# Performance work log

Hardware: AMD Instinct MI355X
Metric: run time of the kernel (lower is better)

## Reference

```python
import jax, jax.numpy as jnp
import numpy as np

PAD_ID, BOS_ID, EOS_ID = 0, 2, 3
NHEAD = 8


def _sincos(T, d):
    pos = jnp.arange(T, dtype=jnp.float32)
    omega = jnp.exp(-jnp.arange(0, d, 2, dtype=jnp.float32) * (np.log(10000.0) / d))
    out = pos[:, None] * omega[None, :]  # [T, d/2]
    return jnp.stack([jnp.sin(out), jnp.cos(out)], axis=2).reshape(T, d)[None]  # [1,T,d]


def _ln(x, g, b, eps=1e-5):
    mu = x.mean(-1, keepdims=True)
    var = ((x - mu) ** 2).mean(-1, keepdims=True)
    return (x - mu) / jnp.sqrt(var + eps) * g + b


def _mha(q_in, kv_in, wqkv, bqkv, wo, bo, mask):
    B, Tq, d = q_in.shape
    Tk = kv_in.shape[1]
    hd = d // NHEAD
    q = q_in @ wqkv[:d].T + bqkv[:d]
    k = kv_in @ wqkv[d:2 * d].T + bqkv[d:2 * d]
    v = kv_in @ wqkv[2 * d:].T + bqkv[2 * d:]
    q = q.reshape(B, Tq, NHEAD, hd).transpose(0, 2, 1, 3)
    k = k.reshape(B, Tk, NHEAD, hd).transpose(0, 2, 1, 3)
    v = v.reshape(B, Tk, NHEAD, hd).transpose(0, 2, 1, 3)
    s = jnp.einsum('bhqd,bhkd->bhqk', q, k) / np.sqrt(hd)
    if mask is not None:
        s = s + mask
    a = jax.nn.softmax(s, axis=-1)
    o = jnp.einsum('bhqk,bhkd->bhqd', a, v).transpose(0, 2, 1, 3).reshape(B, Tq, d)
    return o @ wo.T + bo


def _last_logits(tokens, state, emb_table, qkv_w, qkv_b, out_w, out_b,
                 ffn_w1, ffn_b1, ffn_w2, ffn_b2, ln_g, ln_b):
    T = tokens.shape[1]
    d = emb_table.shape[1]
    x = emb_table[tokens] * np.sqrt(d) + _sincos(T, d)
    mask = jnp.where(jnp.tril(jnp.ones((T, T), bool)), 0.0, -jnp.inf)
    L = qkv_w.shape[0]
    for l in range(L):
        x = _ln(x + _mha(x, x, qkv_w[l, 0], qkv_b[l, 0], out_w[l, 0], out_b[l, 0], mask), ln_g[l, 0], ln_b[l, 0])
        x = _ln(x + _mha(x, state, qkv_w[l, 1], qkv_b[l, 1], out_w[l, 1], out_b[l, 1], None), ln_g[l, 1], ln_b[l, 1])
        h = jax.nn.gelu(x @ ffn_w1[l].T + ffn_b1[l], approximate=False)
        x = _ln(x + h @ ffn_w2[l].T + ffn_b2[l], ln_g[l, 2], ln_b[l, 2])
    return x[:, -1, :] @ emb_table.T  # tied output projection


def setup_inputs() -> dict:
    key = jax.random.key(0)
    ks = jax.random.split(key, 8)
    V, d, L, dff, B, K = 32000, 512, 4, 2048, 8, 64
    s = 0.02
    emb = jax.random.normal(ks[1], (V, d), jnp.float32) * s
    emb = emb.at[PAD_ID].set(0.0)  # padding_idx row is zero
    return {
        'state': jax.random.normal(ks[0], (B, K, d), jnp.float32),
        'emb_table': emb,
        'qkv_w': jax.random.normal(ks[2], (L, 2, 3 * d, d), jnp.float32) * s,
        'qkv_b': jnp.zeros((L, 2, 3 * d), jnp.float32),
        'out_w': jax.random.normal(ks[3], (L, 2, d, d), jnp.float32) * s,
        'out_b': jnp.zeros((L, 2, d), jnp.float32),
        'ffn_w1': jax.random.normal(ks[4], (L, dff, d), jnp.float32) * s,
        'ffn_b1': jnp.zeros((L, dff), jnp.float32),
        'ffn_w2': jax.random.normal(ks[5], (L, d, dff), jnp.float32) * s,
        'ffn_b2': jnp.zeros((L, d), jnp.float32),
        'ln_g': jnp.ones((L, 3, d), jnp.float32),
        'ln_b': jnp.zeros((L, 3, d), jnp.float32),
        'max_length': 16,
        'top_k': 50,
    }


def reference(state, emb_table, qkv_w, qkv_b, out_w, out_b, ffn_w1, ffn_b1,
              ffn_w2, ffn_b2, ln_g, ln_b, max_length, top_k):
    B = state.shape[0]
    generated = jnp.full((B, 1), BOS_ID, dtype=jnp.int32)
    finished = jnp.zeros(B, dtype=bool)
    key = jax.random.key(1)
    temperature = 1.0
    for t in range(max_length):
        # faithful naive recompute: full self+cross attention over generated prefix
        logits = _last_logits(generated, state, emb_table, qkv_w, qkv_b, out_w, out_b,
                              ffn_w1, ffn_b1, ffn_w2, ffn_b2, ln_g, ln_b)
        logits = logits / max(temperature, 1e-8)
        thr = jax.lax.top_k(logits, top_k)[0][:, -1:]
        filt = jnp.where(logits < thr, -jnp.inf, logits)
        nxt = jax.random.categorical(jax.random.fold_in(key, t), filt, axis=-1)
        nxt = jnp.where(finished, PAD_ID, nxt).astype(jnp.int32)
        generated = jnp.concatenate([generated, nxt[:, None]], axis=1)
        finished = finished | (nxt == EOS_ID)
    return generated
```

## Files before the change

### kernel.cpp

```cpp
#include <hip/hip_runtime.h>
#include <math.h>
#include <stdint.h>

#define D     512
#define DFF   2048
#define BB    8
#define NB    2
#define NG    4
#define NH    8
#define HD    64
#define NV    32000
#define NL    4
#define TMAX  17
#define KC    64
#define STEPS 16
#define KTOP  50
#define PAD_ID 0
#define BOS_ID 2
#define EOS_ID 3
#define SCOPE __HIP_MEMORY_SCOPE_AGENT

__device__ __forceinline__ float ld1(const float* p) {
  return __hip_atomic_load(p, __ATOMIC_RELAXED, SCOPE);
}
__device__ __forceinline__ void st1(float* p, float v) {
  __hip_atomic_store(p, v, __ATOMIC_RELAXED, SCOPE);
}
__device__ __forceinline__ float2 ld2(const float* p) {
  union { double d; float2 f; } u;
  u.d = __hip_atomic_load((const double*)p, __ATOMIC_RELAXED, SCOPE);
  return u.f;
}
__device__ __forceinline__ unsigned ldu(const unsigned* p) {
  return __hip_atomic_load(p, __ATOMIC_RELAXED, SCOPE);
}

__device__ __forceinline__ void tf2x32(unsigned k0, unsigned k1, unsigned x0, unsigned x1,
                                       unsigned& o0, unsigned& o1)
{
  unsigned ks2 = k0 ^ k1 ^ 0x1BD11BDAu;
#define TFR(r) { x0 += x1; x1 = (x1 << (r)) | (x1 >> (32 - (r))); x1 ^= x0; }
  x0 += k0; x1 += k1;
  TFR(13) TFR(15) TFR(26) TFR(6)
  x0 += k1;  x1 += ks2 + 1u;
  TFR(17) TFR(29) TFR(16) TFR(24)
  x0 += ks2; x1 += k0 + 2u;
  TFR(13) TFR(15) TFR(26) TFR(6)
  x0 += k0;  x1 += k1 + 3u;
  TFR(17) TFR(29) TFR(16) TFR(24)
  x0 += k1;  x1 += ks2 + 4u;
  TFR(13) TFR(15) TFR(26) TFR(6)
  o0 = x0 + ks2; o1 = x1 + k0 + 5u;
#undef TFR
}

__device__ __forceinline__ float wredf(float v) {
  for (int o = 32; o; o >>= 1) v += __shfl_xor(v, o, 64);
  return v;
}
__device__ __forceinline__ float wredmaxf(float v) {
  for (int o = 32; o; o >>= 1) v = fmaxf(v, __shfl_xor(v, o, 64));
  return v;
}
__device__ __forceinline__ unsigned monok(float f) {
  unsigned u = __float_as_uint(f);
  return (u & 0x80000000u) ? ~u : (u | 0x80000000u);
}

#define DOT8(a0,a1,x0,x1) (a0.x*x0.x + a0.y*x0.y + a0.z*x0.z + a0.w*x0.w + \
                           a1.x*x1.x + a1.y*x1.y + a1.z*x1.z + a1.w*x1.w)

__global__ void init_k(int* toks, unsigned* bars)
{
  int i = threadIdx.x;
  if (i < BB) toks[i * TMAX] = BOS_ID;
  for (int k = i; k < 2048; k += 256) bars[k] = 0u;
}

__global__ void cross_kv_k(const float* __restrict__ state, const float* __restrict__ qkvw,
                           const float* __restrict__ qkvb, float* __restrict__ cK,
                           float* __restrict__ cV)
{
  int gx = blockIdx.x, b = blockIdx.y, tid = threadIdx.x;
  int jblk = gx & 31, kpos = (gx >> 5) & 63, l = gx >> 11;
  int w = tid >> 6, lane = tid & 63;
  __shared__ __align__(16) float xsh[D];
  xsh[tid] = state[((size_t)b * KC + kpos) * D + tid];
  xsh[tid + 256] = state[((size_t)b * KC + kpos) * D + tid + 256];
  __syncthreads();
  for (int i = 0; i < 8; i++) {
    int j = jblk * 32 + w * 8 + i;
    int row = D + j;
    const float4* wr = (const float4*)(qkvw + (((size_t)l * 2 + 1) * (3 * D) + row) * D);
    const float4* x4 = (const float4*)xsh;
    float acc = 0.f;
    for (int e = lane; e < 128; e += 64) {
      float4 a = wr[e], xx = x4[e];
      acc += a.x * xx.x + a.y * xx.y + a.z * xx.z + a.w * xx.w;
    }
    acc = wredf(acc);
    if (lane == 0) {
      float v = acc + qkvb[((size_t)l * 2 + 1) * (3 * D) + row];
      float* dst = (j < D) ? cK : cV;
      int jj = (j < D) ? j : j - D;
      dst[(((size_t)l * BB + b) * KC + kpos) * D + jj] = v;
    }
  }
}

extern "C" __global__ void __launch_bounds__(512, 2)
decode_k(const float* __restrict__ emb, const float* __restrict__ qkv_w,
         const float* __restrict__ qkv_b, const float* __restrict__ out_w,
         const float* __restrict__ out_b, const float* __restrict__ f_w1,
         const float* __restrict__ f_b1, const float* __restrict__ f_w2,
         const float* __restrict__ f_b2, const float* __restrict__ lng,
         const float* __restrict__ lnb,
         const float* __restrict__ cK, const float* __restrict__ cV,
         float* Kc, float* Vc, float* qS, float* q2S,
         float* xt2, float* xt3, float* xt4, float* hB,
         float* xcur, float* lg, unsigned* bars, int* toks)
{
  const int tid = threadIdx.x, bid = blockIdx.x;
  const int xcd = bid & 7;
  const int g2 = xcd >> 1;
  const int half = xcd & 1;
  const int hid = bid >> 3;
  const int gid = hid * 2 + half;
  const int sb = (gid + g2 * 16) & 63;
  const int b0 = g2 * 2, b1 = b0 + 1;
  const int w = tid >> 6, lane = tid & 63;
  const int wb = w >> 2;
  const int ws = w & 3;
  unsigned gp = 0, glp = 0;
  int finished = 0;

  __shared__ __align__(16) unsigned char smem[65280];
  float* F = (float*)smem;
  float* sX1 = F;
  float* sX2 = F + 1024;
  float* sQ  = F + 2048;
  float* sAO = F + 3072;
  float* sS  = F + 4096;
  float* sSP = F + 5184;
  float* sH  = F + 6272;
  float* sRed = F + 10368;
  float* sL  = F;
  unsigned short* key16 = (unsigned short*)smem;
  unsigned* histA = (unsigned*)(smem + 64000);
  unsigned* sKeys = (unsigned*)(smem + 64000);
  unsigned* sMeta = (unsigned*)(smem + 65024);
  float*    sWin  = (float*)(smem + 65056);
  int*      sWix  = (int*)(smem + 65120);

  const float SQD = (float)22.627416997969522;
  const float PEC = (float)(9.210340371976184 / 512.0);
  const float SQRT2 = (float)1.4142135623730951;

  auto gbarg = [&]() {
    asm volatile("s_waitcnt vmcnt(0)" ::: "memory");
    __syncthreads();
    ++gp;
    if (tid == 0) {
      unsigned* c = bars + g2 * 256;
      __hip_atomic_fetch_add(&c[(gid & 3) * 32], 1u, __ATOMIC_RELAXED, SCOPE);
      unsigned tgt = gp * 16u;
      if (gid == 0) {
        for (;;) {
          unsigned s0 = ldu(&c[0]), s1 = ldu(&c[32]), s2 = ldu(&c[64]), s3 = ldu(&c[96]);
          unsigned mn = s0 < s1 ? s0 : s1;
          unsigned mn2 = s2 < s3 ? s2 : s3;
          if ((mn < mn2 ? mn : mn2) >= tgt) break;
          __builtin_amdgcn_s_sleep(1);
        }
        __hip_atomic_store(&c[128], gp, __ATOMIC_RELAXED, SCOPE);
      } else {
        while (ldu(&c[128]) < gp) __builtin_amdgcn_s_sleep(1);
      }
    }
    asm volatile("" ::: "memory");
    __syncthreads();
  };
  auto gbarall = [&]() {
    asm volatile("s_waitcnt vmcnt(0)" ::: "memory");
    __syncthreads();
    ++glp;
    if (tid == 0) {
      unsigned* c = bars + 1024;
      __hip_atomic_fetch_add(&c[(bid & 15) * 32], 1u, __ATOMIC_RELAXED, SCOPE);
      unsigned tgt = glp * 16u;
      if (bid == 0) {
        for (;;) {
          unsigned mn = 0xFFFFFFFFu;
#pragma unroll
          for (int i = 0; i < 16; i++) { unsigned x = ldu(&c[i * 32]); mn = x < mn ? x : mn; }
          if (mn >= tgt) break;
          __builtin_amdgcn_s_sleep(1);
        }
        __hip_atomic_store(&c[576], glp, __ATOMIC_RELAXED, SCOPE);
      } else {
        while (ldu(&c[576]) < glp) __builtin_amdgcn_s_sleep(1);
      }
    }
    asm volatile("" ::: "memory");
    __syncthreads();
  };

  auto ln2 = [&](const float* srcbase, const float* gamma, const float* beta, float* dst) {
    int nb = tid >> 8, e = tid & 255;
    const float* sp = srcbase + (size_t)(b0 + nb) * D;
    float v0 = ld1(sp + e), v1 = ld1(sp + e + 256);
    float s = wredf(v0 + v1);
    if (lane == 0) sRed[w] = s;
    __syncthreads();
    float mu = (sRed[nb*4] + sRed[nb*4+1] + sRed[nb*4+2] + sRed[nb*4+3]) * (1.0f/512.0f);
    __syncthreads();
    float d0 = v0 - mu, d1 = v1 - mu;
    float q = wredf(d0*d0 + d1*d1);
    if (lane == 0) sRed[w] = q;
    __syncthreads();
    float sd = sqrtf((sRed[nb*4] + sRed[nb*4+1] + sRed[nb*4+2] + sRed[nb*4+3]) * (1.0f/512.0f) + 1e-5f);
    dst[nb*512 + e]       = d0 / sd * gamma[e]       + beta[e];
    dst[nb*512 + e + 256] = d1 / sd * gamma[e + 256] + beta[e + 256];
    __syncthreads();
  };

  if (bid < BB) {
    float pe = (tid & 1) ? 1.0f : 0.0f;
    st1(&xcur[bid * D + tid], emb[(size_t)BOS_ID * D + tid] * SQD + pe);
  }
  gbarg();

  for (int t = 0; t < STEPS; ++t) {
    const int T = t + 1;
    for (int l = 0; l < NL; ++l) {
      const float* wqkv0 = qkv_w + ((size_t)l * 2 + 0) * (3 * D) * D;
      const float* bqkv0 = qkv_b + ((size_t)l * 2 + 0) * (3 * D);
      const float* wqkv1 = qkv_w + ((size_t)l * 2 + 1) * (3 * D) * D;
      const float* bqkv1 = qkv_b + ((size_t)l * 2 + 1) * (3 * D);
      const float* wo0 = out_w + ((size_t)l * 2 + 0) * D * D;
      const float* bo0 = out_b + ((size_t)l * 2 + 0) * D;
      const float* wo1 = out_w + ((size_t)l * 2 + 1) * D * D;
      const float* bo1 = out_b + ((size_t)l * 2 + 1) * D;

      if (l == 0) {
        int nb = tid >> 8, e = tid & 255;
        sX1[nb*512 + e]       = ld1(&xcur[(b0 + nb) * D + e]);
        sX1[nb*512 + e + 256] = ld1(&xcur[(b0 + nb) * D + e + 256]);
        __syncthreads();
      } else {
        ln2(xt4, lng + ((size_t)(l - 1) * 3 + 2) * D, lnb + ((size_t)(l - 1) * 3 + 2) * D, sX1);
      }
      {
        const float4* xs4 = (const float4*)(sX1 + wb * 512);
        float4 x0 = xs4[lane], x1v = xs4[lane + 64];
        int jq = sb * 8 + ws * 2;
        int kvb = 512 + sb * 16 + ws * 4;
        float4 qa[2], qb[2], wa[4], wbv[4];
#pragma unroll
        for (int r = 0; r < 2; ++r) {
          const float4* w4 = (const float4*)(wqkv0 + (size_t)(jq + r) * D);
          qa[r] = w4[lane]; qb[r] = w4[lane + 64];
        }
#pragma unroll
        for (int r = 0; r < 4; ++r) {
          const float4* w4 = (const float4*)(wqkv0 + (size_t)(kvb + r) * D);
          wa[r] = w4[lane]; wbv[r] = w4[lane + 64];
        }
        float aq[2], ak[4];
#pragma unroll
        for (int r = 0; r < 2; ++r) aq[r] = DOT8(qa[r], qb[r], x0, x1v);
#pragma unroll
        for (int r = 0; r < 4; ++r) ak[r] = DOT8(wa[r], wbv[r], x0, x1v);
#pragma unroll
        for (int o = 32; o; o >>= 1) {
#pragma unroll
          for (int r = 0; r < 2; ++r) aq[r] += __shfl_xor(aq[r], o, 64);
#pragma unroll
          for (int r = 0; r < 4; ++r) ak[r] += __shfl_xor(ak[r], o, 64);
        }
        if (lane == 0) {
#pragma unroll
          for (int r = 0; r < 2; ++r) {
            int j = jq + r;
            st1(&qS[(size_t)(b0 + wb) * D + j], aq[r] + bqkv0[j]);
          }
#pragma unroll
          for (int r = 0; r < 4; ++r) {
            int j = kvb + r;
            float v = ak[r] + bqkv0[j];
            if (j < 1024)
              st1(&Kc[((((size_t)g2 * NL + l) * NB + wb) * TMAX + t) * D + (j - 512)], v);
            else
              st1(&Vc[((((size_t)g2 * NL + l) * NB + wb) * TMAX + t) * D + (j - 1024)], v);
          }
        }
      }
      gbarg();

      {
        int nb = tid >> 8, e = tid & 255;
        sQ[nb*512 + e]       = ld1(&qS[(b0 + nb) * D + e]);
        sQ[nb*512 + e + 256] = ld1(&qS[(b0 + nb) * D + e + 256]);
      }
      __syncthreads();
      for (int o = tid; o < NB * NH * TMAX; o += 512) {
        int nb = o / (NH * TMAX), rem = o - nb * (NH * TMAX);
        int h = rem / TMAX, k = rem - h * TMAX;
        if (k < T) {
          const float4* Kr = (const float4*)(Kc + ((((size_t)g2 * NL + l) * NB + nb) * TMAX + k) * D + h * HD);
          const float4* q4 = (const float4*)(sQ + nb * 512 + h * HD);
          float sc = 0.f;
#pragma unroll
          for (int e = 0; e < 16; ++e) {
            float4 a = Kr[e], b2 = q4[e];
            sc += a.x * b2.x + a.y * b2.y + a.z * b2.z + a.w * b2.w;
          }
          sS[nb * 544 + h * TMAX + k] = sc * 0.125f;
        }
      }
      __syncthreads();
      for (int rr = w; rr < 16; rr += 8) {
        int nb = rr >> 3, h = rr & 7;
        float v = (lane < T) ? sS[nb * 544 + h * TMAX + lane] : -INFINITY;
        float m = wredmaxf(v);
        float p = (lane < T) ? expf(v - m) : 0.f;
        float den = wredf(p);
        if (lane < T) sSP[nb * 544 + h * TMAX + lane] = p / den;
      }
      __syncthreads();
      for (int o = tid; o < 1024; o += 512) {
        int nb = o >> 9, dd = o & 511, h = dd >> 6, d3 = dd & 63;
        const float* Vb = Vc + ((((size_t)g2 * NL + l) * NB + nb) * TMAX) * D + h * HD + d3;
        float acc = 0.f;
        for (int k = 0; k < T; ++k) acc += sSP[nb * 544 + h * TMAX + k] * Vb[(size_t)k * D];
        sAO[nb * 512 + dd] = acc;
      }
      __syncthreads();
      {
        int jb = sb * 8 + ws * 2;
        const float4* yN = (const float4*)(sAO + wb * 512);
        float4 y0 = yN[lane], y1 = yN[lane + 64];
        float acc[2];
#pragma unroll
        for (int r = 0; r < 2; ++r) {
          const float4* w4 = (const float4*)(wo0 + (size_t)(jb + r) * D);
          float4 a0 = w4[lane], a1 = w4[lane + 64];
          acc[r] = DOT8(a0, a1, y0, y1);
        }
#pragma unroll
        for (int o = 32; o; o >>= 1) {
#pragma unroll
          for (int r = 0; r < 2; ++r) acc[r] += __shfl_xor(acc[r], o, 64);
        }
        if (lane == 0) {
#pragma unroll
          for (int r = 0; r < 2; ++r) {
            int j = jb + r;
            st1(&xt2[(size_t)(b0 + wb) * D + j], acc[r] + bo0[j] + sX1[wb * 512 + j]);
          }
        }
      }
      gbarg();

      ln2(xt2, lng + ((size_t)l * 3 + 0) * D, lnb + ((size_t)l * 3 + 0) * D, sX2);
      {
        int jb = sb * 8 + ws * 2;
        const float4* yN = (const float4*)(sX2 + wb * 512);
        float4 y0 = yN[lane], y1 = yN[lane + 64];
        float acc[2];
#pragma unroll
        for (int r = 0; r < 2; ++r) {
          const float4* w4 = (const float4*)(wqkv1 + (size_t)(jb + r) * D);
          float4 a0 = w4[lane], a1 = w4[lane + 64];
          acc[r] = DOT8(a0, a1, y0, y1);
        }
#pragma unroll
        for (int o = 32; o; o >>= 1) {
#pragma unroll
          for (int r = 0; r < 2; ++r) acc[r] += __shfl_xor(acc[r], o, 64);
        }
        if (lane == 0) {
#pragma unroll
          for (int r = 0; r < 2; ++r) {
            int j = jb + r;
            st1(&q2S[(size_t)(b0 + wb) * D + j], acc[r] + bqkv1[j]);
          }
        }
      }
      gbarg();

      {
        int nb = tid >> 8, e = tid & 255;
        sQ[nb*512 + e]       = ld1(&q2S[(b0 + nb) * D + e]);
        sQ[nb*512 + e + 256] = ld1(&q2S[(b0 + nb) * D + e + 256]);
      }
      __syncthreads();
      for (int o = tid; o < 1024; o += 512) {
        int nb = o >> 9, dd = o & 511, h = dd >> 6, k = dd & 63;
        const float4* Kr = (const float4*)(cK + (((size_t)l * BB + b0 + nb) * KC + k) * D + h * HD);
        const float4* q4 = (const float4*)(sQ + nb * 512 + h * HD);
        float sc = 0.f;
#pragma unroll
        for (int e = 0; e < 16; ++e) {
          float4 a = Kr[e], b2 = q4[e];
          sc += a.x * b2.x + a.y * b2.y + a.z * b2.z + a.w * b2.w;
        }
        sS[nb * 512 + dd] = sc * 0.125f;
      }
      __syncthreads();
      for (int rr = w; rr < 16; rr += 8) {
        int nb = rr >> 3, h = rr & 7;
        float v = sS[nb * 512 + h * 64 + lane];
        float m = wredmaxf(v);
        float p = expf(v - m);
        float den = wredf(p);
        sSP[nb * 512 + h * 64 + lane] = p / den;
      }
      __syncthreads();
      for (int o = tid; o < 1024; o += 512) {
        int nb = o >> 9, dd = o & 511, h = dd >> 6, d3 = dd & 63;
        const float* Vb = cV + (((size_t)l * BB + b0 + nb) * KC) * D + h * HD + d3;
        float acc = 0.f;
        for (int k = 0; k < KC; ++k) acc += sSP[nb * 512 + h * 64 + k] * Vb[(size_t)k * D];
        sAO[nb * 512 + dd] = acc;
      }
      __syncthreads();
      {
        int jb = sb * 8 + ws * 2;
        const float4* yN = (const float4*)(sAO + wb * 512);
        float4 y0 = yN[lane], y1 = yN[lane + 64];
        float acc[2];
#pragma unroll
        for (int r = 0; r < 2; ++r) {
          const float4* w4 = (const float4*)(wo1 + (size_t)(jb + r) * D);
          float4 a0 = w4[lane], a1 = w4[lane + 64];
          acc[r] = DOT8(a0, a1, y0, y1);
        }
#pragma unroll
        for (int o = 32; o; o >>= 1) {
#pragma unroll
          for (int r = 0; r < 2; ++r) acc[r] += __shfl_xor(acc[r], o, 64);
        }
        if (lane == 0) {
#pragma unroll
          for (int r = 0; r < 2; ++r) {
            int j = jb + r;
            st1(&xt3[(size_t)(b0 + wb) * D + j], acc[r] + bo1[j] + sX2[wb * 512 + j]);
          }
        }
      }
      gbarg();

      ln2(xt3, lng + ((size_t)l * 3 + 1) * D, lnb + ((size_t)l * 3 + 1) * D, sX1);
      {
        const float4* xs4 = (const float4*)(sX1 + wb * 512);
        float4 x0 = xs4[lane], x1v = xs4[lane + 64];
        for (int pass = 0; pass < 2; ++pass) {
          int jb = sb * 32 + ws * 8 + pass * 4;
          float4 wa[4], wbv[4];
#pragma unroll
          for (int r = 0; r < 4; ++r) {
            const float4* w4 = (const float4*)(f_w1 + (size_t)l * DFF * D + (size_t)(jb + r) * D);
            wa[r] = w4[lane]; wbv[r] = w4[lane + 64];
          }
          float acc[4];
#pragma unroll
          for (int r = 0; r < 4; ++r) acc[r] = DOT8(wa[r], wbv[r], x0, x1v);
#pragma unroll
          for (int o = 32; o; o >>= 1) {
#pragma unroll
            for (int r = 0; r < 4; ++r) acc[r] += __shfl_xor(acc[r], o, 64);
          }
          if (lane == 0) {
#pragma unroll
            for (int r = 0; r < 4; ++r) {
              int j = jb + r;
              float v = acc[r] + f_b1[(size_t)l * DFF + j];
              v = v * (erff(v / SQRT2) + 1.0f) / 2.0f;
              st1(&hB[(size_t)(b0 + wb) * DFF + j], v);
            }
          }
        }
      }
      gbarg();

      for (int ii = tid; ii < 2048; ii += 512) {
        int nbb = ii >> 10, ee = (ii & 1023) * 2;
        float2 v = ld2(&hB[(size_t)(b0 + nbb) * DFF + ee]);
        sH[nbb * 2048 + ee] = v.x; sH[nbb * 2048 + ee + 1] = v.y;
      }
      __syncthreads();
      {
        int jb = sb * 8 + ws * 2;
        const float4* hN = (const float4*)(sH + wb * 2048);
        float acc[2];
#pragma unroll
        for (int r = 0; r < 2; ++r) {
          const float4* w4 = (const float4*)(f_w2 + (size_t)l * D * DFF + (size_t)(jb + r) * DFF);
          float a = 0.f;
#pragma unroll
          for (int e = 0; e < 8; ++e) {
            float4 aw0 = w4[lane + e * 64];
            float4 hh0 = hN[lane + e * 64];
            a += aw0.x * hh0.x + aw0.y * hh0.y + aw0.z * hh0.z + aw0.w * hh0.w;
          }
          acc[r] = a;
        }
#pragma unroll
        for (int o = 32; o; o >>= 1) {
#pragma unroll
          for (int r = 0; r < 2; ++r) acc[r] += __shfl_xor(acc[r], o, 64);
        }
        if (lane == 0) {
#pragma unroll
          for (int r = 0; r < 2; ++r) {
            int j = jb + r;
            st1(&xt4[(size_t)(b0 + wb) * D + j], acc[r] + f_b2[(size_t)l * D + j] + sX1[wb * 512 + j]);
          }
        }
      }
      if (l < NL - 1) gbarg(); else gbarall();
    }

    for (int ii = tid; ii < 2048; ii += 512) {
      float2 v = ld2(&xt4[2 * ii]);
      sL[2 * ii] = v.x; sL[2 * ii + 1] = v.y;
    }
    __syncthreads();
    {
      int b = w;
      float vals[8]; float s = 0.f;
#pragma unroll
      for (int e = 0; e < 8; ++e) { vals[e] = sL[b * D + lane + e * 64]; s += vals[e]; }
      s = wredf(s);
      float mu = s * (1.0f / 512.0f);
      float q = 0.f;
#pragma unroll
      for (int e = 0; e < 8; ++e) { float d0 = vals[e] - mu; q += d0 * d0; }
      q = wredf(q);
      float sd = sqrtf(q * (1.0f / 512.0f) + 1e-5f);
      const float* ga = lng + 11 * D;
      const float* be = lnb + 11 * D;
#pragma unroll
      for (int e = 0; e < 8; ++e)
        sL[b * D + lane + e * 64] = (vals[e] - mu) / sd * ga[lane + e * 64] + be[lane + e * 64];
    }
    __syncthreads();
    for (int i = w; i < 125; i += 8) {
      int v = i * 256 + bid;
      const float4* er = (const float4*)(emb + (size_t)v * D);
      float4 e0 = er[lane], e1 = er[lane + 64];
      float acc[8];
#pragma unroll
      for (int b = 0; b < 8; b++) {
        const float4* x4 = (const float4*)(sL + b * D);
        float4 x0 = x4[lane], x1v = x4[lane + 64];
        acc[b] = DOT8(e0, e1, x0, x1v);
      }
#pragma unroll
      for (int o = 32; o; o >>= 1) {
#pragma unroll
        for (int b = 0; b < 8; b++) acc[b] += __shfl_xor(acc[b], o, 64);
      }
      if (lane == 0) {
#pragma unroll
        for (int b = 0; b < 8; b++) st1(&lg[(size_t)b * NV + v], acc[b]);
      }
    }
    gbarall();

    if (bid < BB) {
      int b = bid;
      if (tid < 256) histA[tid] = 0u;
      __syncthreads();
      for (int v2 = tid; v2 < NV / 2; v2 += 512) {
        float2 f = ld2(&lg[(size_t)b * NV + 2 * v2]);
        unsigned u0 = monok(f.x), u1 = monok(f.y);
        key16[2 * v2] = (unsigned short)(u0 >> 16);
        key16[2 * v2 + 1] = (unsigned short)(u1 >> 16);
        atomicAdd(&histA[u0 >> 24], 1u);
        atomicAdd(&histA[u1 >> 24], 1u);
      }
      __syncthreads();
      if (tid == 0) {
        unsigned k = KTOP, cum = 0;
        for (int bin = 255; bin >= 0; bin--) {
          cum += histA[bin];
          if (cum >= k) { sMeta[0] = (unsigned)bin; sMeta[1] = k - (cum - histA[bin]); break; }
        }
      }
      __syncthreads();
      unsigned selHi = sMeta[0], rem1 = sMeta[1];
      if (tid < 256) histA[tid] = 0u;
      __syncthreads();
      for (int v = tid; v < NV; v += 512) {
        unsigned k16 = key16[v];
        if ((k16 >> 8) == selHi) atomicAdd(&histA[k16 & 255u], 1u);
      }
      __syncthreads();
      if (tid == 0) {
        unsigned k = rem1, cum = 0;
        for (int bin = 255; bin >= 0; bin--) {
          cum += histA[bin];
          if (cum >= k) { sMeta[2] = (selHi << 8) | (unsigned)bin; sMeta[1] = k - (cum - histA[bin]); break; }
        }
        sMeta[3] = 0u;
      }
      __syncthreads();
      unsigned P16 = sMeta[2], rem2 = sMeta[1];
      for (int v = tid; v < NV; v += 512) {
        if (key16[v] == (unsigned short)P16) {
          unsigned i = atomicAdd(&sMeta[3], 1u);
          if (i < 256) sKeys[i] = monok(ld1(&lg[(size_t)b * NV + v]));
        }
      }
      __syncthreads();
      if (tid == 0) {
        unsigned n = sMeta[3]; if (n > 256) n = 256;
        unsigned thr = 0;
        for (unsigned it = 0; it < rem2; ++it) {
          unsigned bestk = 0; int bj = 0;
          for (unsigned jx = 0; jx < n; jx++)
            if (sKeys[jx] > bestk) { bestk = sKeys[jx]; bj = (int)jx; }
          thr = bestk;
          sKeys[bj] = 0u;
        }
        sMeta[5] = (thr & 0x80000000u) ? (thr ^ 0x80000000u) : ~thr;
      }
      __syncthreads();
      float th = __uint_as_float(sMeta[5]);
      unsigned k0, k1;
      tf2x32(0u, 1u, 0u, (unsigned)t, k0, k1);
      float best = -INFINITY; int bi = NV;
      for (int v = tid; v < NV; v += 512) {
        if (key16[v] >= (unsigned short)P16) {
          float lo = ld1(&lg[(size_t)b * NV + v]);
          if (lo >= th) {
            unsigned o0, o1;
            tf2x32(k0, k1, 0u, (unsigned)(b * NV + v), o0, o1);
            unsigned bits = o0 ^ o1;
            unsigned ub = (bits >> 9) | 0x3f800000u;
            float fu = __uint_as_float(ub) - 1.0f;
            const float TINY = 1.17549435e-38f;
            float u = fu * (1.0f - TINY) + TINY;
            u = fmaxf(TINY, u);
            float gmb = -logf(-logf(u));
            float s = lo + gmb;
            if (s > best || (s == best && v < bi)) { best = s; bi = v; }
          }
        }
      }
      for (int o = 32; o; o >>= 1) {
        float ob = __shfl_xor(best, o, 64); int ox = __shfl_xor(bi, o, 64);
        if (ob > best || (ob == best && ox < bi)) { best = ob; bi = ox; }
      }
      if (lane == 0) { sWin[w] = best; sWix[w] = bi; }
      __syncthreads();
      if (tid == 0) {
        float bb = sWin[0]; int bx = sWix[0];
        for (int i2 = 1; i2 < 8; i2++) {
          if (sWin[i2] > bb || (sWin[i2] == bb && sWix[i2] < bx)) { bb = sWin[i2]; bx = sWix[i2]; }
        }
        int tok = bx;
        if (finished) tok = PAD_ID;
        toks[b * TMAX + t + 1] = tok;
        if (tok == EOS_ID) finished = 1;
        sMeta[4] = (unsigned)tok;
      }
      __syncthreads();
      {
        int tok = (int)sMeta[4];
        float omega = expf(-(float)(tid & ~1) * PEC);
        float val = (float)(t + 1) * omega;
        float pe = (tid & 1) ? cosf(val) : sinf(val);
        st1(&xcur[b * D + tid], emb[(size_t)tok * D + tid] * SQD + pe);
      }
    }
    gbarg();
  }
}

extern "C" void kernel_launch(void* const* d_in, const int* in_sizes, int n_in,
                              void* d_out, int out_size, void* d_ws, size_t ws_size,
                              hipStream_t stream)
{
  const float* state = (const float*)d_in[0];
  const float* emb   = (const float*)d_in[1];
  const float* qkv_w = (const float*)d_in[2];
  const float* qkv_b = (const float*)d_in[3];
  const float* out_w = (const float*)d_in[4];
  const float* out_b = (const float*)d_in[5];
  const float* f_w1  = (const float*)d_in[6];
  const float* f_b1  = (const float*)d_in[7];
  const float* f_w2  = (const float*)d_in[8];
  const float* f_b2  = (const float*)d_in[9];
  const float* lng   = (const float*)d_in[10];
  const float* lnb   = (const float*)d_in[11];

  float* ws = (float*)d_ws;
  float* cK   = ws;
  float* cV   = cK + (size_t)NL * BB * KC * D;
  float* Kc   = cV + (size_t)NL * BB * KC * D;
  float* Vc   = Kc + (size_t)8 * NL * NB * TMAX * D;
  float* qS   = Vc + (size_t)8 * NL * NB * TMAX * D;
  float* q2S  = qS + BB * D;
  float* xt2  = q2S + BB * D;
  float* xt3  = xt2 + BB * D;
  float* xt4  = xt3 + BB * D;
  float* hB   = xt4 + BB * D;
  float* xcur = hB + BB * DFF;
  float* lg   = xcur + BB * D;
  unsigned* bars = (unsigned*)(lg + (size_t)BB * NV);

  int* toks = (int*)d_out;

  init_k<<<1, 256, 0, stream>>>(toks, bars);
  cross_kv_k<<<dim3(NL * KC * 32, BB), 256, 0, stream>>>(state, qkv_w, qkv_b, cK, cV);
  decode_k<<<256, 512, 0, stream>>>(emb, qkv_w, qkv_b, out_w, out_b,
                                    f_w1, f_b1, f_w2, f_b2, lng, lnb,
                                    cK, cV, Kc, Vc, qS, q2S,
                                    xt2, xt3, xt4, hB, xcur, lg, bars, toks);
}
```

Measured before the change: 4.960 ms.

## Prefetch stage weights before barrier-dependent work and spin without sleep

Each stage's weight rows (QKV, out-proj, FFN first pass) are now loaded into registers before the LayerNorm, attention, or activation reads that depend on the preceding grid barrier. The global-memory weight latency can then overlap with the reductions and attention math. The grid barrier spin loops also drop s_sleep, to cut wake-up latency at each barrier. The cost is higher register pressure and more polling traffic on the barrier counters.

```diff
diff --git a/kernel.cpp b/kernel.cpp
--- a/kernel.cpp
+++ b/kernel.cpp
@@ -170,11 +170,10 @@
           unsigned mn = s0 < s1 ? s0 : s1;
           unsigned mn2 = s2 < s3 ? s2 : s3;
           if ((mn < mn2 ? mn : mn2) >= tgt) break;
-          __builtin_amdgcn_s_sleep(1);
         }
         __hip_atomic_store(&c[128], gp, __ATOMIC_RELAXED, SCOPE);
       } else {
-        while (ldu(&c[128]) < gp) __builtin_amdgcn_s_sleep(1);
+        while (ldu(&c[128]) < gp) {}
       }
     }
     asm volatile("" ::: "memory");
@@ -194,11 +193,10 @@
 #pragma unroll
           for (int i = 0; i < 16; i++) { unsigned x = ldu(&c[i * 32]); mn = x < mn ? x : mn; }
           if (mn >= tgt) break;
-          __builtin_amdgcn_s_sleep(1);
         }
         __hip_atomic_store(&c[576], glp, __ATOMIC_RELAXED, SCOPE);
       } else {
-        while (ldu(&c[576]) < glp) __builtin_amdgcn_s_sleep(1);
+        while (ldu(&c[576]) < glp) {}
       }
     }
     asm volatile("" ::: "memory");
@@ -242,17 +240,7 @@
       const float* wo1 = out_w + ((size_t)l * 2 + 1) * D * D;
       const float* bo1 = out_b + ((size_t)l * 2 + 1) * D;
 
-      if (l == 0) {
-        int nb = tid >> 8, e = tid & 255;
-        sX1[nb*512 + e]       = ld1(&xcur[(b0 + nb) * D + e]);
-        sX1[nb*512 + e + 256] = ld1(&xcur[(b0 + nb) * D + e + 256]);
-        __syncthreads();
-      } else {
-        ln2(xt4, lng + ((size_t)(l - 1) * 3 + 2) * D, lnb + ((size_t)(l - 1) * 3 + 2) * D, sX1);
-      }
       {
-        const float4* xs4 = (const float4*)(sX1 + wb * 512);
-        float4 x0 = xs4[lane], x1v = xs4[lane + 64];
         int jq = sb * 8 + ws * 2;
         int kvb = 512 + sb * 16 + ws * 4;
         float4 qa[2], qb[2], wa[4], wbv[4];
@@ -266,6 +254,16 @@
           const float4* w4 = (const float4*)(wqkv0 + (size_t)(kvb + r) * D);
           wa[r] = w4[lane]; wbv[r] = w4[lane + 64];
         }
+        if (l == 0) {
+          int nb = tid >> 8, e = tid & 255;
+          sX1[nb*512 + e]       = ld1(&xcur[(b0 + nb) * D + e]);
+          sX1[nb*512 + e + 256] = ld1(&xcur[(b0 + nb) * D + e + 256]);
+          __syncthreads();
+        } else {
+          ln2(xt4, lng + ((size_t)(l - 1) * 3 + 2) * D, lnb + ((size_t)(l - 1) * 3 + 2) * D, sX1);
+        }
+        const float4* xs4 = (const float4*)(sX1 + wb * 512);
+        float4 x0 = xs4[lane], x1v = xs4[lane + 64];
         float aq[2], ak[4];
 #pragma unroll
         for (int r = 0; r < 2; ++r) aq[r] = DOT8(qa[r], qb[r], x0, x1v);
@@ -298,16 +296,118 @@
       gbarg();
 
       {
-        int nb = tid >> 8, e = tid & 255;
-        sQ[nb*512 + e]       = ld1(&qS[(b0 + nb) * D + e]);
-        sQ[nb*512 + e + 256] = ld1(&qS[(b0 + nb) * D + e + 256]);
-      }
-      __syncthreads();
-      for (int o = tid; o < NB * NH * TMAX; o += 512) {
-        int nb = o / (NH * TMAX), rem = o - nb * (NH * TMAX);
-        int h = rem / TMAX, k = rem - h * TMAX;
-        if (k < T) {
-          const float4* Kr = (const float4*)(Kc + ((((size_t)g2 * NL + l) * NB + nb) * TMAX + k) * D + h * HD);
+        int jb = sb * 8 + ws * 2;
+        float4 oa[2], ob[2];
+#pragma unroll
+        for (int r = 0; r < 2; ++r) {
+          const float4* w4 = (const float4*)(wo0 + (size_t)(jb + r) * D);
+          oa[r] = w4[lane]; ob[r] = w4[lane + 64];
+        }
+        {
+          int nb = tid >> 8, e = tid & 255;
+          sQ[nb*512 + e]       = ld1(&qS[(b0 + nb) * D + e]);
+          sQ[nb*512 + e + 256] = ld1(&qS[(b0 + nb) * D + e + 256]);
+        }
+        __syncthreads();
+        for (int o = tid; o < NB * NH * TMAX; o += 512) {
+          int nb = o / (NH * TMAX), rem = o - nb * (NH * TMAX);
+          int h = rem / TMAX, k = rem - h * TMAX;
+          if (k < T) {
+            const float4* Kr = (const float4*)(Kc + ((((size_t)g2 * NL + l) * NB + nb) * TMAX + k) * D + h * HD);
+            const float4* q4 = (const float4*)(sQ + nb * 512 + h * HD);
+            float sc = 0.f;
+#pragma unroll
+            for (int e = 0; e < 16; ++e) {
+              float4 a = Kr[e], b2 = q4[e];
+              sc += a.x * b2.x + a.y * b2.y + a.z * b2.z + a.w * b2.w;
+            }
+            sS[nb * 544 + h * TMAX + k] = sc * 0.125f;
+          }
+        }
+        __syncthreads();
+        for (int rr = w; rr < 16; rr += 8) {
+          int nb = rr >> 3, h = rr & 7;
+          float v = (lane < T) ? sS[nb * 544 + h * TMAX + lane] : -INFINITY;
+          float m = wredmaxf(v);
+          float p = (lane < T) ? expf(v - m) : 0.f;
+          float den = wredf(p);
+          if (lane < T) sSP[nb * 544 + h * TMAX + lane] = p / den;
+        }
+        __syncthreads();
+        for (int o = tid; o < 1024; o += 512) {
+          int nb = o >> 9, dd = o & 511, h = dd >> 6, d3 = dd & 63;
+          const float* Vb = Vc + ((((size_t)g2 * NL + l) * NB + nb) * TMAX) * D + h * HD + d3;
+          float acc = 0.f;
+          for (int k = 0; k < T; ++k) acc += sSP[nb * 544 + h * TMAX + k] * Vb[(size_t)k * D];
+          sAO[nb * 512 + dd] = acc;
+        }
+        __syncthreads();
+        const float4* yN = (const float4*)(sAO + wb * 512);
+        float4 y0 = yN[lane], y1 = yN[lane + 64];
+        float acc[2];
+#pragma unroll
+        for (int r = 0; r < 2; ++r) acc[r] = DOT8(oa[r], ob[r], y0, y1);
+#pragma unroll
+        for (int o = 32; o; o >>= 1) {
+#pragma unroll
+          for (int r = 0; r < 2; ++r) acc[r] += __shfl_xor(acc[r], o, 64);
+        }
+        if (lane == 0) {
+#pragma unroll
+          for (int r = 0; r < 2; ++r) {
+            int j = jb + r;
+            st1(&xt2[(size_t)(b0 + wb) * D + j], acc[r] + bo0[j] + sX1[wb * 512 + j]);
+          }
+        }
+      }
+      gbarg();
+
+      {
+        int jb = sb * 8 + ws * 2;
+        float4 qa[2], qb[2];
+#pragma unroll
+        for (int r = 0; r < 2; ++r) {
+          const float4* w4 = (const float4*)(wqkv1 + (size_t)(jb + r) * D);
+          qa[r] = w4[lane]; qb[r] = w4[lane + 64];
+        }
+        ln2(xt2, lng + ((size_t)l * 3 + 0) * D, lnb + ((size_t)l * 3 + 0) * D, sX2);
+        const float4* yN = (const float4*)(sX2 + wb * 512);
+        float4 y0 = yN[lane], y1 = yN[lane + 64];
+        float acc[2];
+#pragma unroll
+        for (int r = 0; r < 2; ++r) acc[r] = DOT8(qa[r], qb[r], y0, y1);
+#pragma unroll
+        for (int o = 32; o; o >>= 1) {
+#pragma unroll
+          for (int r = 0; r < 2; ++r) acc[r] += __shfl_xor(acc[r], o, 64);
+        }
+        if (lane == 0) {
+#pragma unroll
+          for (int r = 0; r < 2; ++r) {
+            int j = jb + r;
+            st1(&q2S[(size_t)(b0 + wb) * D + j], acc[r] + bqkv1[j]);
+          }
+        }
+      }
+      gbarg();
+
+      {
+        int jb = sb * 8 + ws * 2;
+        float4 oa[2], ob[2];
+#pragma unroll
+        for (int r = 0; r < 2; ++r) {
+          const float4* w4 = (const float4*)(wo1 + (size_t)(jb + r) * D);
+          oa[r] = w4[lane]; ob[r] = w4[lane + 64];
+        }
+        {
+          int nb = tid >> 8, e = tid & 255;
+          sQ[nb*512 + e]       = ld1(&q2S[(b0 + nb) * D + e]);
+          sQ[nb*512 + e + 256] = ld1(&q2S[(b0 + nb) * D + e + 256]);
+        }
+        __syncthreads();
+        for (int o = tid; o < 1024; o += 512) {
+          int nb = o >> 9, dd = o & 511, h = dd >> 6, k = dd & 63;
+          const float4* Kr = (const float4*)(cK + (((size_t)l * BB + b0 + nb) * KC + k) * D + h * HD);
           const float4* q4 = (const float4*)(sQ + nb * 512 + h * HD);
           float sc = 0.f;
 #pragma unroll
@@ -315,127 +415,31 @@
             float4 a = Kr[e], b2 = q4[e];
             sc += a.x * b2.x + a.y * b2.y + a.z * b2.z + a.w * b2.w;
           }
-          sS[nb * 544 + h * TMAX + k] = sc * 0.125f;
-        }
-      }
-      __syncthreads();
-      for (int rr = w; rr < 16; rr += 8) {
-        int nb = rr >> 3, h = rr & 7;
-        float v = (lane < T) ? sS[nb * 544 + h * TMAX + lane] : -INFINITY;
-        float m = wredmaxf(v);
-        float p = (lane < T) ? expf(v - m) : 0.f;
-        float den = wredf(p);
-        if (lane < T) sSP[nb * 544 + h * TMAX + lane] = p / den;
-      }
-      __syncthreads();
-      for (int o = tid; o < 1024; o += 512) {
-        int nb = o >> 9, dd = o & 511, h = dd >> 6, d3 = dd & 63;
-        const float* Vb = Vc + ((((size_t)g2 * NL + l) * NB + nb) * TMAX) * D + h * HD + d3;
-        float acc = 0.f;
-        for (int k = 0; k < T; ++k) acc += sSP[nb * 544 + h * TMAX + k] * Vb[(size_t)k * D];
-        sAO[nb * 512 + dd] = acc;
-      }
-      __syncthreads();
-      {
-        int jb = sb * 8 + ws * 2;
+          sS[nb * 512 + dd] = sc * 0.125f;
+        }
+        __syncthreads();
+        for (int rr = w; rr < 16; rr += 8) {
+          int nb = rr >> 3, h = rr & 7;
+          float v = sS[nb * 512 + h * 64 + lane];
+          float m = wredmaxf(v);
+          float p = expf(v - m);
+          float den = wredf(p);
+          sSP[nb * 512 + h * 64 + lane] = p / den;
+        }
+        __syncthreads();
+        for (int o = tid; o < 1024; o += 512) {
+          int nb = o >> 9, dd = o & 511, h = dd >> 6, d3 = dd & 63;
+          const float* Vb = cV + (((size_t)l * BB + b0 + nb) * KC) * D + h * HD + d3;
+          float acc = 0.f;
+          for (int k = 0; k < KC; ++k) acc += sSP[nb * 512 + h * 64 + k] * Vb[(size_t)k * D];
+          sAO[nb * 512 + dd] = acc;
+        }
+        __syncthreads();
         const float4* yN = (const float4*)(sAO + wb * 512);
         float4 y0 = yN[lane], y1 = yN[lane + 64];
         float acc[2];
 #pragma unroll
-        for (int r = 0; r < 2; ++r) {
-          const float4* w4 = (const float4*)(wo0 + (size_t)(jb + r) * D);
-          float4 a0 = w4[lane], a1 = w4[lane + 64];
-          acc[r] = DOT8(a0, a1, y0, y1);
-        }
-#pragma unroll
-        for (int o = 32; o; o >>= 1) {
-#pragma unroll
-          for (int r = 0; r < 2; ++r) acc[r] += __shfl_xor(acc[r], o, 64);
-        }
-        if (lane == 0) {
-#pragma unroll
-          for (int r = 0; r < 2; ++r) {
-            int j = jb + r;
-            st1(&xt2[(size_t)(b0 + wb) * D + j], acc[r] + bo0[j] + sX1[wb * 512 + j]);
-          }
-        }
-      }
-      gbarg();
-
-      ln2(xt2, lng + ((size_t)l * 3 + 0) * D, lnb + ((size_t)l * 3 + 0) * D, sX2);
-      {
-        int jb = sb * 8 + ws * 2;
-        const float4* yN = (const float4*)(sX2 + wb * 512);
-        float4 y0 = yN[lane], y1 = yN[lane + 64];
-        float acc[2];
-#pragma unroll
-        for (int r = 0; r < 2; ++r) {
-          const float4* w4 = (const float4*)(wqkv1 + (size_t)(jb + r) * D);
-          float4 a0 = w4[lane], a1 = w4[lane + 64];
-          acc[r] = DOT8(a0, a1, y0, y1);
-        }
-#pragma unroll
-        for (int o = 32; o; o >>= 1) {
-#pragma unroll
-          for (int r = 0; r < 2; ++r) acc[r] += __shfl_xor(acc[r], o, 64);
-        }
-        if (lane == 0) {
-#pragma unroll
-          for (int r = 0; r < 2; ++r) {
-            int j = jb + r;
-            st1(&q2S[(size_t)(b0 + wb) * D + j], acc[r] + bqkv1[j]);
-          }
-        }
-      }
-      gbarg();
-
-      {
-        int nb = tid >> 8, e = tid & 255;
-        sQ[nb*512 + e]       = ld1(&q2S[(b0 + nb) * D + e]);
-        sQ[nb*512 + e + 256] = ld1(&q2S[(b0 + nb) * D + e + 256]);
-      }
-      __syncthreads();
-      for (int o = tid; o < 1024; o += 512) {
-        int nb = o >> 9, dd = o & 511, h = dd >> 6, k = dd & 63;
-        const float4* Kr = (const float4*)(cK + (((size_t)l * BB + b0 + nb) * KC + k) * D + h * HD);
-        const float4* q4 = (const float4*)(sQ + nb * 512 + h * HD);
-        float sc = 0.f;
-#pragma unroll
-        for (int e = 0; e < 16; ++e) {
-          float4 a = Kr[e], b2 = q4[e];
-          sc += a.x * b2.x + a.y * b2.y + a.z * b2.z + a.w * b2.w;
-        }
-        sS[nb * 512 + dd] = sc * 0.125f;
-      }
-      __syncthreads();
-      for (int rr = w; rr < 16; rr += 8) {
-        int nb = rr >> 3, h = rr & 7;
-        float v = sS[nb * 512 + h * 64 + lane];
-        float m = wredmaxf(v);
-        float p = expf(v - m);
-        float den = wredf(p);
-        sSP[nb * 512 + h * 64 + lane] = p / den;
-      }
-      __syncthreads();
-      for (int o = tid; o < 1024; o += 512) {
-        int nb = o >> 9, dd = o & 511, h = dd >> 6, d3 = dd & 63;
-        const float* Vb = cV + (((size_t)l * BB + b0 + nb) * KC) * D + h * HD + d3;
-        float acc = 0.f;
-        for (int k = 0; k < KC; ++k) acc += sSP[nb * 512 + h * 64 + k] * Vb[(size_t)k * D];
-        sAO[nb * 512 + dd] = acc;
-      }
-      __syncthreads();
-      {
-        int jb = sb * 8 + ws * 2;
-        const float4* yN = (const float4*)(sAO + wb * 512);
-        float4 y0 = yN[lane], y1 = yN[lane + 64];
-        float acc[2];
-#pragma unroll
-        for (int r = 0; r < 2; ++r) {
-          const float4* w4 = (const float4*)(wo1 + (size_t)(jb + r) * D);
-          float4 a0 = w4[lane], a1 = w4[lane + 64];
-          acc[r] = DOT8(a0, a1, y0, y1);
-        }
+        for (int r = 0; r < 2; ++r) acc[r] = DOT8(oa[r], ob[r], y0, y1);
 #pragma unroll
         for (int o = 32; o; o >>= 1) {
 #pragma unroll
@@ -451,12 +455,38 @@
       }
       gbarg();
 
-      ln2(xt3, lng + ((size_t)l * 3 + 1) * D, lnb + ((size_t)l * 3 + 1) * D, sX1);
       {
+        int jb0 = sb * 32 + ws * 8;
+        float4 pa[4], pb[4];
+#pragma unroll
+        for (int r = 0; r < 4; ++r) {
+          const float4* w4 = (const float4*)(f_w1 + (size_t)l * DFF * D + (size_t)(jb0 + r) * D);
+          pa[r] = w4[lane]; pb[r] = w4[lane + 64];
+        }
+        ln2(xt3, lng + ((size_t)l * 3 + 1) * D, lnb + ((size_t)l * 3 + 1) * D, sX1);
         const float4* xs4 = (const float4*)(sX1 + wb * 512);
         float4 x0 = xs4[lane], x1v = xs4[lane + 64];
-        for (int pass = 0; pass < 2; ++pass) {
-          int jb = sb * 32 + ws * 8 + pass * 4;
+        {
+          float acc[4];
+#pragma unroll
+          for (int r = 0; r < 4; ++r) acc[r] = DOT8(pa[r], pb[r], x0, x1v);
+#pragma unroll
+          for (int o = 32; o; o >>= 1) {
+#pragma unroll
+            for (int r = 0; r < 4; ++r) acc[r] += __shfl_xor(acc[r], o, 64);
+          }
+          if (lane == 0) {
+#pragma unroll
+            for (int r = 0; r < 4; ++r) {
+              int j = jb0 + r;
+              float v = acc[r] + f_b1[(size_t)l * DFF + j];
+              v = v * (erff(v / SQRT2) + 1.0f) / 2.0f;
+              st1(&hB[(size_t)(b0 + wb) * DFF + j], v);
+            }
+          }
+        }
+        {
+          int jb = jb0 + 4;
           float4 wa[4], wbv[4];
 #pragma unroll
           for (int r = 0; r < 4; ++r) {
```

Result: no change. 5.032 ms (+1.5%).
